# Kernel optimization log

Measured on AMD Instinct MI355X. Metric: run time of the kernel, lower is better.

The kernel has to match this reference:

```python
import jax, jax.numpy as jnp
import numpy as np

DIM = 128
NUM_HEADS = 4
HEAD_DIM = DIM // NUM_HEADS
WS = 8            # window size (square)
SHIFT = 4         # shift size
SCALE = HEAD_DIM ** -0.5
WIN_AREA = WS * WS


def _rel_pos_index(wh, ww):
    coords = np.stack(np.meshgrid(np.arange(wh), np.arange(ww), indexing='ij'))  # (2,wh,ww)
    flat = coords.reshape(2, -1)
    rel = flat[:, :, None] - flat[:, None, :]          # (2,S,S)
    rel = rel.transpose(1, 2, 0).astype(np.int64)
    rel[:, :, 0] += wh - 1
    rel[:, :, 1] += ww - 1
    rel[:, :, 0] *= 2 * ww - 1
    return jnp.asarray(rel.sum(-1))                    # (S,S)

_REL_IDX = _rel_pos_index(WS, WS)


def setup_inputs() -> dict:
    key = jax.random.key(0)
    ks = jax.random.split(key, 6)
    B, C, U, V, H, W = 2, DIM, 5, 5, 64, 64
    return {
        'x': jax.random.normal(ks[0], (B, C, U, V, H, W), dtype=jnp.float32),
        'qkv_w': jax.random.normal(ks[1], (3 * DIM, DIM), dtype=jnp.float32) * 0.02,
        'qkv_b': jax.random.normal(ks[2], (3 * DIM,), dtype=jnp.float32) * 0.02,
        'proj_w': jax.random.normal(ks[3], (DIM, DIM), dtype=jnp.float32) * 0.02,
        'proj_b': jax.random.normal(ks[4], (DIM,), dtype=jnp.float32) * 0.02,
        'rpb_table': jax.random.normal(ks[5], ((2 * WS - 1) ** 2, NUM_HEADS), dtype=jnp.float32) * 0.02,
    }


def reference(x, qkv_w, qkv_b, proj_w, proj_b, proj_bias_unused=None, **_):
    # kept signature explicit below; see wrapper
    raise NotImplementedError


def reference(x, qkv_w, qkv_b, proj_w, proj_b, rpb_table):
    B, C, U, V, H, W = x.shape
    Hn, Wn = H // WS, W // WS
    S = WIN_AREA

    # cyclic shift (torch.roll with shifts (SHIFT,SHIFT) on dims (-1,-2))
    xs = jnp.roll(x, (SHIFT, SHIFT), axis=(-1, -2))

    # window partition: B C U V (Hn wv) (Wn wh) -> (B U V Hn Wn) (wv wh) C
    xw = xs.reshape(B, C, U, V, Hn, WS, Wn, WS)
    xw = xw.transpose(0, 2, 3, 4, 6, 5, 7, 1)          # B U V Hn Wn wv wh C
    xw = xw.reshape(-1, S, C)                          # (nW, S, C)

    # qkv projection (torch Linear: x @ W.T + b)
    qkv = xw @ qkv_w.T + qkv_b                         # (nW, S, 3C)
    nW = qkv.shape[0]
    qkv = qkv.reshape(nW, S, NUM_HEADS, 3 * HEAD_DIM).transpose(0, 2, 1, 3)  # (nW,h,S,3d)
    q, k, v = jnp.split(qkv, 3, axis=-1)               # each (nW,h,S,d)

    attn = jnp.einsum('bhqd,bhkd->bhqk', q * SCALE, k)  # (nW,h,S,S)
    bias = rpb_table[_REL_IDX]                          # (S,S,h)
    attn = attn + bias.transpose(2, 0, 1)[None]         # (1,h,S,S) broadcast
    attn = jax.nn.softmax(attn, axis=-1)

    out = jnp.einsum('bhqk,bhkd->bhqd', attn, v)        # (nW,h,S,d)
    out = out.transpose(0, 2, 1, 3).reshape(nW, S, C)   # merge heads
    out = out @ proj_w.T + proj_b

    # window un-partition back to B C U V H W
    out = out.reshape(B, U, V, Hn, Wn, WS, WS, C)
    out = out.transpose(0, 7, 1, 2, 3, 5, 4, 6)         # B C U V Hn wv Wn wh
    out = out.reshape(B, C, U, V, H, W)

    # reverse shift
    return jnp.roll(out, (-SHIFT, -SHIFT), axis=(-1, -2))
```

## Files before the change

kernel.cpp:

```cpp
#include <hip/hip_runtime.h>

#define NH 4
#define HD 32
#define ST 64
#define CD 128
#define IMG 102400
#define VHW 20480
#define HW_ 4096
#define SCALE_ 0.17677669529663687f

typedef __attribute__((ext_vector_type(8))) short bf16x8;
typedef __attribute__((ext_vector_type(4))) float f32x4;

__device__ __forceinline__ short f2bf(float f) {
    unsigned int u = __float_as_uint(f);
    u = (u + 0x7FFF + ((u >> 16) & 1)) >> 16;
    return (short)u;
}

__global__ void cvt_w_kernel(const float* __restrict__ qkv_w,
                             const float* __restrict__ proj_w,
                             short* __restrict__ wq,
                             short* __restrict__ wp) {
    int i = blockIdx.x * 256 + threadIdx.x;
    if (i < 49152) wq[i] = f2bf(qkv_w[i]);
    else           wp[i - 49152] = f2bf(proj_w[i - 49152]);
}


__global__ __launch_bounds__(256, 2)
void win_attn_mfma(const float* __restrict__ x,
                   const short* __restrict__ wq,
                   const float* __restrict__ qkv_b,
                   const short* __restrict__ wp,
                   const float* __restrict__ proj_b,
                   const float* __restrict__ rpb,
                   float* __restrict__ out) {
    __shared__ __align__(16) short smem[38400];

    const int t    = threadIdx.x;
    const int h    = __builtin_amdgcn_readfirstlane(t >> 6);
    const int ln   = t & 15;
    const int quad = (t >> 4) & 3;
    const int tok  = t & 63;

    const int wid = (blockIdx.x & 7) * 400 + (blockIdx.x >> 3);

    const int wn = wid & 7, hn = (wid >> 3) & 7;
    int rem = wid >> 6;
    const int v = rem % 5; rem /= 5;
    const int u = rem % 5;
    const int b = rem / 5;

    const int hh = (((hn << 3) + (tok >> 3)) - 4) & 63;
    const int ww = (((wn << 3) + (tok & 7)) - 4) & 63;
    const long pix = (long)b * (CD * IMG) + u * VHW + v * HW_ + hh * 64 + ww;

    short* X  = smem;
    short* Qh = smem + 8704 + h * 5120;
    short* Kh = Qh + 2560;
    short* Ph = Qh;
    short* Vh = smem + 29184 + h * 2304;

    float xr[32];
    #pragma unroll
    for (int kh = 0; kh < 4; ++kh)
        #pragma unroll
        for (int j = 0; j < 8; ++j)
            xr[kh * 8 + j] = x[pix + (long)(kh * 32 + h * 8 + j) * IMG];
    #pragma unroll
    for (int kh = 0; kh < 4; ++kh) {
        bf16x8 pk;
        #pragma unroll
        for (int j = 0; j < 8; ++j) pk[j] = f2bf(xr[kh * 8 + j]);
        *(bf16x8*)(X + tok * 136 + kh * 32 + h * 8) = pk;
    }
    __syncthreads();

    f32x4 acc[6][4];
    #pragma unroll
    for (int n = 0; n < 6; ++n)
        #pragma unroll
        for (int mt = 0; mt < 4; ++mt) acc[n][mt] = (f32x4){0.f, 0.f, 0.f, 0.f};

    #pragma unroll
    for (int kh = 0; kh < 4; ++kh) {
        bf16x8 af[4];
        #pragma unroll
        for (int mt = 0; mt < 4; ++mt)
            af[mt] = *(const bf16x8*)(X + (mt * 16 + ln) * 136 + kh * 32 + quad * 8);
        #pragma unroll
        for (int n = 0; n < 6; ++n) {
            bf16x8 bf = *(const bf16x8*)(wq + (h * 96 + n * 16 + ln) * 128 + kh * 32 + quad * 8);
            #pragma unroll
            for (int mt = 0; mt < 4; ++mt)
                acc[n][mt] = __builtin_amdgcn_mfma_f32_16x16x32_bf16(af[mt], bf, acc[n][mt], 0, 0, 0);
        }
    }

    #pragma unroll
    for (int n = 0; n < 6; ++n) {
        const float bias = qkv_b[h * 96 + n * 16 + ln];
        #pragma unroll
        for (int mt = 0; mt < 4; ++mt)
            #pragma unroll
            for (int r = 0; r < 4; ++r) {
                const float val = acc[n][mt][r] + bias;
                const int tk = mt * 16 + quad * 4 + r;
                if (n < 2)      Qh[tk * 40 + n * 16 + ln] = f2bf(val * SCALE_);
                else if (n < 4) Kh[tk * 40 + (n - 2) * 16 + ln] = f2bf(val);
                else            Vh[((n - 4) * 16 + ln) * 72 + tk] = f2bf(val);
            }
    }

    bf16x8 aq[4], bk[4];
    #pragma unroll
    for (int mt = 0; mt < 4; ++mt) aq[mt] = *(const bf16x8*)(Qh + (mt * 16 + ln) * 40 + quad * 8);
    #pragma unroll
    for (int nt = 0; nt < 4; ++nt) bk[nt] = *(const bf16x8*)(Kh + (nt * 16 + ln) * 40 + quad * 8);
    f32x4 s[4][4];
    #pragma unroll
    for (int mt = 0; mt < 4; ++mt)
        #pragma unroll
        for (int nt = 0; nt < 4; ++nt) {
            f32x4 z = (f32x4){0.f, 0.f, 0.f, 0.f};
            s[mt][nt] = __builtin_amdgcn_mfma_f32_16x16x32_bf16(aq[mt], bk[nt], z, 0, 0, 0);
        }

    #pragma unroll
    for (int nt = 0; nt < 4; ++nt) {
        const int kcol = nt * 16 + ln;
        const int ik = kcol >> 3, jk = kcol & 7;
        #pragma unroll
        for (int mt = 0; mt < 4; ++mt)
            #pragma unroll
            for (int r = 0; r < 4; ++r) {
                const int q = mt * 16 + quad * 4 + r;
                const int ridx = ((q >> 3) - ik + 7) * 15 + ((q & 7) - jk + 7);
                s[mt][nt][r] += rpb[ridx * 4 + h];
            }
    }

    float inv[4][4];
    #pragma unroll
    for (int mt = 0; mt < 4; ++mt)
        #pragma unroll
        for (int r = 0; r < 4; ++r) {
            float m = fmaxf(fmaxf(s[mt][0][r], s[mt][1][r]), fmaxf(s[mt][2][r], s[mt][3][r]));
            #pragma unroll
            for (int msk = 1; msk < 16; msk <<= 1) m = fmaxf(m, __shfl_xor(m, msk, 64));
            float sum = 0.f;
            #pragma unroll
            for (int nt = 0; nt < 4; ++nt) {
                float e = __expf(s[mt][nt][r] - m);
                s[mt][nt][r] = e;
                sum += e;
            }
            #pragma unroll
            for (int msk = 1; msk < 16; msk <<= 1) sum += __shfl_xor(sum, msk, 64);
            inv[mt][r] = 1.f / sum;
            const int q = mt * 16 + quad * 4 + r;
            #pragma unroll
            for (int nt = 0; nt < 4; ++nt)
                Ph[q * 72 + nt * 16 + ln] = f2bf(s[mt][nt][r]);
        }

    f32x4 oa[4][2];
    #pragma unroll
    for (int mt = 0; mt < 4; ++mt)
        #pragma unroll
        for (int nt = 0; nt < 2; ++nt) oa[mt][nt] = (f32x4){0.f, 0.f, 0.f, 0.f};
    #pragma unroll
    for (int kt = 0; kt < 2; ++kt) {
        bf16x8 ap[4], bv[2];
        #pragma unroll
        for (int mt = 0; mt < 4; ++mt)
            ap[mt] = *(const bf16x8*)(Ph + (mt * 16 + ln) * 72 + kt * 32 + quad * 8);
        #pragma unroll
        for (int nt = 0; nt < 2; ++nt)
            bv[nt] = *(const bf16x8*)(Vh + (nt * 16 + ln) * 72 + kt * 32 + quad * 8);
        #pragma unroll
        for (int mt = 0; mt < 4; ++mt)
            #pragma unroll
            for (int nt = 0; nt < 2; ++nt)
                oa[mt][nt] = __builtin_amdgcn_mfma_f32_16x16x32_bf16(ap[mt], bv[nt], oa[mt][nt], 0, 0, 0);
    }

    __syncthreads();
    short* O = smem;
    #pragma unroll
    for (int mt = 0; mt < 4; ++mt)
        #pragma unroll
        for (int nt = 0; nt < 2; ++nt)
            #pragma unroll
            for (int r = 0; r < 4; ++r)
                O[(mt * 16 + quad * 4 + r) * 136 + h * 32 + nt * 16 + ln] =
                    f2bf(oa[mt][nt][r] * inv[mt][r]);
    __syncthreads();

    f32x4 pa[4][2];
    #pragma unroll
    for (int mt = 0; mt < 4; ++mt)
        #pragma unroll
        for (int nt = 0; nt < 2; ++nt) pa[mt][nt] = (f32x4){0.f, 0.f, 0.f, 0.f};
    #pragma unroll
    for (int kt = 0; kt < 4; ++kt) {
        bf16x8 ao[4], bw[2];
        #pragma unroll
        for (int mt = 0; mt < 4; ++mt)
            ao[mt] = *(const bf16x8*)(O + (mt * 16 + ln) * 136 + kt * 32 + quad * 8);
        #pragma unroll
        for (int nt = 0; nt < 2; ++nt)
            bw[nt] = *(const bf16x8*)(wp + (h * 32 + nt * 16 + ln) * 128 + kt * 32 + quad * 8);
        #pragma unroll
        for (int mt = 0; mt < 4; ++mt)
            #pragma unroll
            for (int nt = 0; nt < 2; ++nt)
                pa[mt][nt] = __builtin_amdgcn_mfma_f32_16x16x32_bf16(ao[mt], bw[nt], pa[mt][nt], 0, 0, 0);
    }
    float pb[2];
    #pragma unroll
    for (int nt = 0; nt < 2; ++nt) pb[nt] = proj_b[h * 32 + nt * 16 + ln];

    __syncthreads();
    float* F = (float*)smem;
    #pragma unroll
    for (int mt = 0; mt < 4; ++mt)
        #pragma unroll
        for (int nt = 0; nt < 2; ++nt)
            #pragma unroll
            for (int r = 0; r < 4; ++r)
                F[(h * 32 + nt * 16 + ln) * 65 + mt * 16 + quad * 4 + r] = pa[mt][nt][r] + pb[nt];
    __syncthreads();

    #pragma unroll
    for (int j = 0; j < 32; ++j) {
        const int c = h * 32 + j;
        out[pix + (long)c * IMG] = F[c * 65 + tok];
    }
}

__global__ __launch_bounds__(256, 1)
void win_attn_fallback(const float* __restrict__ x,
                       const float* __restrict__ wQKV,
                       const float* __restrict__ qkv_b,
                       const float* __restrict__ wP,
                       const float* __restrict__ proj_b,
                       const float* __restrict__ rpb,
                       float* __restrict__ out) {
    __shared__ __align__(16) float k_lds[NH * ST * HD];
    __shared__ __align__(16) float v_lds[NH * ST * HD];
    const int t = threadIdx.x;
    const int h = __builtin_amdgcn_readfirstlane(t >> 6);
    const int l = t & 63;
    const int wid = blockIdx.x;
    const int wn = wid & 7, hn = (wid >> 3) & 7;
    int rem = wid >> 6;
    const int v = rem % 5; rem /= 5;
    const int u = rem % 5;
    const int b = rem / 5;
    const int hh = (((hn << 3) + (l >> 3)) - 4) & 63;
    const int ww = (((wn << 3) + (l & 7)) - 4) & 63;
    const int pix = b * (NH * HD * IMG) + u * VHW + v * HW_ + hh * 64 + ww;
    float q[HD], kk[HD], vv[HD];
    const float* bq = qkv_b + h * 96;
    #pragma unroll
    for (int d = 0; d < HD; ++d) { q[d] = bq[d]; kk[d] = bq[32 + d]; vv[d] = bq[64 + d]; }
    for (int c = 0; c < CD; ++c) {
        float xv = x[pix + c * IMG];
        const float* wc = wQKV + h * 96 * CD + c;
        #pragma unroll
        for (int d = 0; d < HD; ++d) {
            q[d]  = fmaf(xv, wc[d * CD], q[d]);
            kk[d] = fmaf(xv, wc[(32 + d) * CD], kk[d]);
            vv[d] = fmaf(xv, wc[(64 + d) * CD], vv[d]);
        }
    }
    float* kr = k_lds + (h * ST + l) * HD;
    float* vr = v_lds + (h * ST + l) * HD;
    #pragma unroll
    for (int d = 0; d < HD; ++d) { kr[d] = kk[d]; vr[d] = vv[d]; }
    __syncthreads();
    const float* kh2 = k_lds + h * ST * HD;
    const float* vh2 = v_lds + h * ST * HD;
    const int iq = l >> 3, jq = l & 7;
    float m = -1e30f;
    for (int sk = 0; sk < ST; ++sk) {
        const float* kp = kh2 + sk * HD;
        float a2 = 0.f;
        #pragma unroll
        for (int d = 0; d < HD; ++d) a2 = fmaf(q[d], kp[d], a2);
        int ridx = (iq - (sk >> 3) + 7) * 15 + (jq - (sk & 7) + 7);
        m = fmaxf(m, fmaf(a2, SCALE_, rpb[ridx * 4 + h]));
    }
    float o[HD];
    #pragma unroll
    for (int d = 0; d < HD; ++d) o[d] = 0.f;
    float ssum = 0.f;
    for (int sk = 0; sk < ST; ++sk) {
        const float* kp = kh2 + sk * HD;
        float a2 = 0.f;
        #pragma unroll
        for (int d = 0; d < HD; ++d) a2 = fmaf(q[d], kp[d], a2);
        int ridx = (iq - (sk >> 3) + 7) * 15 + (jq - (sk & 7) + 7);
        float e = __expf(fmaf(a2, SCALE_, rpb[ridx * 4 + h]) - m);
        ssum += e;
        const float* vp = vh2 + sk * HD;
        #pragma unroll
        for (int d = 0; d < HD; ++d) o[d] = fmaf(e, vp[d], o[d]);
    }
    const float inv = 1.f / ssum;
    __syncthreads();
    float* ot = k_lds;
    #pragma unroll
    for (int d = 0; d < HD; ++d) ot[(h * HD + d) * ST + l] = o[d] * inv;
    __syncthreads();
    float o2[HD];
    const float* pb2 = proj_b + h * HD;
    #pragma unroll
    for (int j = 0; j < HD; ++j) o2[j] = pb2[j];
    for (int c = 0; c < CD; ++c) {
        float xv = ot[c * ST + l];
        const float* pc = wP + h * HD * CD + c;
        #pragma unroll
        for (int j = 0; j < HD; ++j) o2[j] = fmaf(xv, pc[j * CD], o2[j]);
    }
    float* ob = out + pix;
    #pragma unroll
    for (int j = 0; j < HD; ++j) ob[(h * HD + j) * IMG] = o2[j];
}

extern "C" void kernel_launch(void* const* d_in, const int* in_sizes, int n_in,
                              void* d_out, int out_size, void* d_ws, size_t ws_size,
                              hipStream_t stream) {
    const float* x      = (const float*)d_in[0];
    const float* qkv_w  = (const float*)d_in[1];
    const float* qkv_b  = (const float*)d_in[2];
    const float* proj_w = (const float*)d_in[3];
    const float* proj_b = (const float*)d_in[4];
    const float* rpb    = (const float*)d_in[5];
    float* out = (float*)d_out;

    const int nW = 2 * 5 * 5 * 8 * 8;
    const size_t need = (size_t)(49152 + 16384) * sizeof(short);

    if (ws_size >= need) {
        short* wq = (short*)d_ws;
        short* wp = wq + 49152;
        cvt_w_kernel<<<256, 256, 0, stream>>>(qkv_w, proj_w, wq, wp);
        win_attn_mfma<<<nW, 256, 0, stream>>>(x, wq, qkv_b, wp, proj_b, rpb, out);
    } else {
        win_attn_fallback<<<nW, 256, 0, stream>>>(x, qkv_w, qkv_b, proj_w, proj_b, rpb, out);
    }
}
```

Before: 314.4 us.

## Vectorize window I/O with float4, prefetch weight fragments, precompute dense bias table

Global loads and stores of each window now use float4 accesses along the W dimension: each thread handles 4 consecutive pixels for 8 channels, replacing scalar per-channel accesses. The bf16 weight fragments for the QKV and output projections are loaded into registers up front so their latency overlaps the input loads and softmax. The relative-position bias is expanded once into a dense per-head 64x64 table in the conversion kernel, which removes index arithmetic and gathers from the softmax path. The register arrays holding the weight fragments raise register pressure and may reduce occupancy or cause spills.

```diff
diff --git a/kernel.cpp b/kernel.cpp
--- a/kernel.cpp
+++ b/kernel.cpp
@@ -20,21 +20,30 @@
 
 __global__ void cvt_w_kernel(const float* __restrict__ qkv_w,
                              const float* __restrict__ proj_w,
+                             const float* __restrict__ rpb,
                              short* __restrict__ wq,
-                             short* __restrict__ wp) {
+                             short* __restrict__ wp,
+                             float* __restrict__ bt) {
     int i = blockIdx.x * 256 + threadIdx.x;
     if (i < 49152) wq[i] = f2bf(qkv_w[i]);
-    else           wp[i - 49152] = f2bf(proj_w[i - 49152]);
-}
-
-
+    else if (i < 65536) wp[i - 49152] = f2bf(proj_w[i - 49152]);
+    else if (i < 81920) {
+        int j = i - 65536;
+        int hh = j >> 12, q = (j >> 6) & 63, k = j & 63;
+        int ridx = ((q >> 3) - (k >> 3) + 7) * 15 + ((q & 7) - (k & 7) + 7);
+        bt[j] = rpb[ridx * 4 + hh];
+    }
+}
+
+
+template <bool DB>
 __global__ __launch_bounds__(256, 2)
 void win_attn_mfma(const float* __restrict__ x,
                    const short* __restrict__ wq,
                    const float* __restrict__ qkv_b,
                    const short* __restrict__ wp,
                    const float* __restrict__ proj_b,
-                   const float* __restrict__ rpb,
+                   const float* __restrict__ bias,
                    float* __restrict__ out) {
     __shared__ __align__(16) short smem[38400];
 
@@ -42,19 +51,22 @@
     const int h    = __builtin_amdgcn_readfirstlane(t >> 6);
     const int ln   = t & 15;
     const int quad = (t >> 4) & 3;
-    const int tok  = t & 63;
+
+    const int s    = t & 15;
+    const int cb   = t >> 4;
+    const int gr   = s >> 1;
+    const int ghalf= s & 1;
 
     const int wid = (blockIdx.x & 7) * 400 + (blockIdx.x >> 3);
-
     const int wn = wid & 7, hn = (wid >> 3) & 7;
     int rem = wid >> 6;
     const int v = rem % 5; rem /= 5;
     const int u = rem % 5;
     const int b = rem / 5;
 
-    const int hh = (((hn << 3) + (tok >> 3)) - 4) & 63;
-    const int ww = (((wn << 3) + (tok & 7)) - 4) & 63;
-    const long pix = (long)b * (CD * IMG) + u * VHW + v * HW_ + hh * 64 + ww;
+    const int hh_r = (((hn << 3) + gr) - 4) & 63;
+    const int ww0  = (((wn << 3) + ghalf * 4) - 4) & 63;
+    const long pixrs = (long)b * (CD * IMG) + u * VHW + v * HW_ + hh_r * 64 + ww0;
 
     short* X  = smem;
     short* Qh = smem + 8704 + h * 5120;
@@ -62,18 +74,24 @@
     short* Ph = Qh;
     short* Vh = smem + 29184 + h * 2304;
 
-    float xr[32];
+    float4 xv[8];
+    #pragma unroll
+    for (int j = 0; j < 8; ++j)
+        xv[j] = *(const float4*)(x + pixrs + (long)(cb * 8 + j) * IMG);
+
+    bf16x8 wqf[24];
     #pragma unroll
     for (int kh = 0; kh < 4; ++kh)
         #pragma unroll
-        for (int j = 0; j < 8; ++j)
-            xr[kh * 8 + j] = x[pix + (long)(kh * 32 + h * 8 + j) * IMG];
-    #pragma unroll
-    for (int kh = 0; kh < 4; ++kh) {
+        for (int n = 0; n < 6; ++n)
+            wqf[kh * 6 + n] = *(const bf16x8*)(wq + (h * 96 + n * 16 + ln) * 128 + kh * 32 + quad * 8);
+
+    #pragma unroll
+    for (int px = 0; px < 4; ++px) {
         bf16x8 pk;
         #pragma unroll
-        for (int j = 0; j < 8; ++j) pk[j] = f2bf(xr[kh * 8 + j]);
-        *(bf16x8*)(X + tok * 136 + kh * 32 + h * 8) = pk;
+        for (int j = 0; j < 8; ++j) pk[j] = f2bf(((const float*)&xv[j])[px]);
+        *(bf16x8*)(X + (gr * 8 + ghalf * 4 + px) * 136 + cb * 8) = pk;
     }
     __syncthreads();
 
@@ -90,22 +108,20 @@
         for (int mt = 0; mt < 4; ++mt)
             af[mt] = *(const bf16x8*)(X + (mt * 16 + ln) * 136 + kh * 32 + quad * 8);
         #pragma unroll
-        for (int n = 0; n < 6; ++n) {
-            bf16x8 bf = *(const bf16x8*)(wq + (h * 96 + n * 16 + ln) * 128 + kh * 32 + quad * 8);
+        for (int n = 0; n < 6; ++n)
             #pragma unroll
             for (int mt = 0; mt < 4; ++mt)
-                acc[n][mt] = __builtin_amdgcn_mfma_f32_16x16x32_bf16(af[mt], bf, acc[n][mt], 0, 0, 0);
-        }
+                acc[n][mt] = __builtin_amdgcn_mfma_f32_16x16x32_bf16(af[mt], wqf[kh * 6 + n], acc[n][mt], 0, 0, 0);
     }
 
     #pragma unroll
     for (int n = 0; n < 6; ++n) {
-        const float bias = qkv_b[h * 96 + n * 16 + ln];
+        const float bias_v = qkv_b[h * 96 + n * 16 + ln];
         #pragma unroll
         for (int mt = 0; mt < 4; ++mt)
             #pragma unroll
             for (int r = 0; r < 4; ++r) {
-                const float val = acc[n][mt][r] + bias;
+                const float val = acc[n][mt][r] + bias_v;
                 const int tk = mt * 16 + quad * 4 + r;
                 if (n < 2)      Qh[tk * 40 + n * 16 + ln] = f2bf(val * SCALE_);
                 else if (n < 4) Kh[tk * 40 + (n - 2) * 16 + ln] = f2bf(val);
@@ -118,27 +134,40 @@
     for (int mt = 0; mt < 4; ++mt) aq[mt] = *(const bf16x8*)(Qh + (mt * 16 + ln) * 40 + quad * 8);
     #pragma unroll
     for (int nt = 0; nt < 4; ++nt) bk[nt] = *(const bf16x8*)(Kh + (nt * 16 + ln) * 40 + quad * 8);
-    f32x4 s[4][4];
+    f32x4 sm[4][4];
     #pragma unroll
     for (int mt = 0; mt < 4; ++mt)
         #pragma unroll
         for (int nt = 0; nt < 4; ++nt) {
             f32x4 z = (f32x4){0.f, 0.f, 0.f, 0.f};
-            s[mt][nt] = __builtin_amdgcn_mfma_f32_16x16x32_bf16(aq[mt], bk[nt], z, 0, 0, 0);
+            sm[mt][nt] = __builtin_amdgcn_mfma_f32_16x16x32_bf16(aq[mt], bk[nt], z, 0, 0, 0);
         }
 
-    #pragma unroll
-    for (int nt = 0; nt < 4; ++nt) {
-        const int kcol = nt * 16 + ln;
-        const int ik = kcol >> 3, jk = kcol & 7;
+    if (DB) {
+        const float* bt = bias + h * 4096;
         #pragma unroll
         for (int mt = 0; mt < 4; ++mt)
             #pragma unroll
             for (int r = 0; r < 4; ++r) {
-                const int q = mt * 16 + quad * 4 + r;
-                const int ridx = ((q >> 3) - ik + 7) * 15 + ((q & 7) - jk + 7);
-                s[mt][nt][r] += rpb[ridx * 4 + h];
+                const int qi = mt * 16 + quad * 4 + r;
+                #pragma unroll
+                for (int nt = 0; nt < 4; ++nt)
+                    sm[mt][nt][r] += bt[qi * 64 + nt * 16 + ln];
             }
+    } else {
+        #pragma unroll
+        for (int nt = 0; nt < 4; ++nt) {
+            const int kcol = nt * 16 + ln;
+            const int ik = kcol >> 3, jk = kcol & 7;
+            #pragma unroll
+            for (int mt = 0; mt < 4; ++mt)
+                #pragma unroll
+                for (int r = 0; r < 4; ++r) {
+                    const int q = mt * 16 + quad * 4 + r;
+                    const int ridx = ((q >> 3) - ik + 7) * 15 + ((q & 7) - jk + 7);
+                    sm[mt][nt][r] += bias[ridx * 4 + h];
+                }
+        }
     }
 
     float inv[4][4];
@@ -146,14 +175,14 @@
     for (int mt = 0; mt < 4; ++mt)
         #pragma unroll
         for (int r = 0; r < 4; ++r) {
-            float m = fmaxf(fmaxf(s[mt][0][r], s[mt][1][r]), fmaxf(s[mt][2][r], s[mt][3][r]));
+            float m = fmaxf(fmaxf(sm[mt][0][r], sm[mt][1][r]), fmaxf(sm[mt][2][r], sm[mt][3][r]));
             #pragma unroll
             for (int msk = 1; msk < 16; msk <<= 1) m = fmaxf(m, __shfl_xor(m, msk, 64));
             float sum = 0.f;
             #pragma unroll
             for (int nt = 0; nt < 4; ++nt) {
-                float e = __expf(s[mt][nt][r] - m);
-                s[mt][nt][r] = e;
+                float e = __expf(sm[mt][nt][r] - m);
+                sm[mt][nt][r] = e;
                 sum += e;
             }
             #pragma unroll
@@ -162,8 +191,15 @@
             const int q = mt * 16 + quad * 4 + r;
             #pragma unroll
             for (int nt = 0; nt < 4; ++nt)
-                Ph[q * 72 + nt * 16 + ln] = f2bf(s[mt][nt][r]);
+                Ph[q * 72 + nt * 16 + ln] = f2bf(sm[mt][nt][r]);
         }
+
+    bf16x8 wpf[8];
+    #pragma unroll
+    for (int kt = 0; kt < 4; ++kt)
+        #pragma unroll
+        for (int nt = 0; nt < 2; ++nt)
+            wpf[kt * 2 + nt] = *(const bf16x8*)(wp + (h * 32 + nt * 16 + ln) * 128 + kt * 32 + quad * 8);
 
     f32x4 oa[4][2];
     #pragma unroll
@@ -205,38 +241,36 @@
         for (int nt = 0; nt < 2; ++nt) pa[mt][nt] = (f32x4){0.f, 0.f, 0.f, 0.f};
     #pragma unroll
     for (int kt = 0; kt < 4; ++kt) {
-        bf16x8 ao[4], bw[2];
+        bf16x8 ao[4];
         #pragma unroll
         for (int mt = 0; mt < 4; ++mt)
             ao[mt] = *(const bf16x8*)(O + (mt * 16 + ln) * 136 + kt * 32 + quad * 8);
         #pragma unroll
+        for (int mt = 0; mt < 4; ++mt)
+            #pragma unroll
+            for (int nt = 0; nt < 2; ++nt)
+                pa[mt][nt] = __builtin_amdgcn_mfma_f32_16x16x32_bf16(ao[mt], wpf[kt * 2 + nt], pa[mt][nt], 0, 0, 0);
+    }
+    float pb[2];
+    #pragma unroll
+    for (int nt = 0; nt < 2; ++nt) pb[nt] = proj_b[h * 32 + nt * 16 + ln];
+
+    __syncthreads();
+    float* F = (float*)smem;
+    #pragma unroll
+    for (int mt = 0; mt < 4; ++mt)
+        #pragma unroll
         for (int nt = 0; nt < 2; ++nt)
-            bw[nt] = *(const bf16x8*)(wp + (h * 32 + nt * 16 + ln) * 128 + kt * 32 + quad * 8);
-        #pragma unroll
-        for (int mt = 0; mt < 4; ++mt)
-            #pragma unroll
-            for (int nt = 0; nt < 2; ++nt)
-                pa[mt][nt] = __builtin_amdgcn_mfma_f32_16x16x32_bf16(ao[mt], bw[nt], pa[mt][nt], 0, 0, 0);
-    }
-    float pb[2];
-    #pragma unroll
-    for (int nt = 0; nt < 2; ++nt) pb[nt] = proj_b[h * 32 + nt * 16 + ln];
-
-    __syncthreads();
-    float* F = (float*)smem;
-    #pragma unroll
-    for (int mt = 0; mt < 4; ++mt)
-        #pragma unroll
-        for (int nt = 0; nt < 2; ++nt)
             #pragma unroll
             for (int r = 0; r < 4; ++r)
-                F[(h * 32 + nt * 16 + ln) * 65 + mt * 16 + quad * 4 + r] = pa[mt][nt][r] + pb[nt];
-    __syncthreads();
-
-    #pragma unroll
-    for (int j = 0; j < 32; ++j) {
-        const int c = h * 32 + j;
-        out[pix + (long)c * IMG] = F[c * 65 + tok];
+                F[(h * 32 + nt * 16 + ln) * 68 + mt * 16 + quad * 4 + r] = pa[mt][nt][r] + pb[nt];
+    __syncthreads();
+
+    #pragma unroll
+    for (int j = 0; j < 8; ++j) {
+        const int c = cb * 8 + j;
+        float4 f4 = *(const float4*)(F + c * 68 + (gr * 8 + ghalf * 4));
+        *(float4*)(out + pixrs + (long)c * IMG) = f4;
     }
 }
 
@@ -342,13 +376,20 @@
     float* out = (float*)d_out;
 
     const int nW = 2 * 5 * 5 * 8 * 8;
-    const size_t need = (size_t)(49152 + 16384) * sizeof(short);
-
-    if (ws_size >= need) {
-        short* wq = (short*)d_ws;
-        short* wp = wq + 49152;
-        cvt_w_kernel<<<256, 256, 0, stream>>>(qkv_w, proj_w, wq, wp);
-        win_attn_mfma<<<nW, 256, 0, stream>>>(x, wq, qkv_b, wp, proj_b, rpb, out);
+    const size_t need_w  = (size_t)(49152 + 16384) * sizeof(short);
+    const size_t need_db = need_w + (size_t)16384 * sizeof(float);
+
+    if (ws_size >= need_db) {
+        short* wqs = (short*)d_ws;
+        short* wps = wqs + 49152;
+        float* bt  = (float*)(wqs + 65536);
+        cvt_w_kernel<<<320, 256, 0, stream>>>(qkv_w, proj_w, rpb, wqs, wps, bt);
+        win_attn_mfma<true><<<nW, 256, 0, stream>>>(x, wqs, qkv_b, wps, proj_b, bt, out);
+    } else if (ws_size >= need_w) {
+        short* wqs = (short*)d_ws;
+        short* wps = wqs + 49152;
+        cvt_w_kernel<<<256, 256, 0, stream>>>(qkv_w, proj_w, rpb, wqs, wps, nullptr);
+        win_attn_mfma<false><<<nW, 256, 0, stream>>>(x, wqs, qkv_b, wps, proj_b, rpb, out);
     } else {
         win_attn_fallback<<<nW, 256, 0, stream>>>(x, qkv_w, qkv_b, proj_w, proj_b, rpb, out);
     }
```

Measured after the change: 298.5 us. 1.05x faster.
